# Kernel optimization log

Hardware: AMD Instinct MI355X
Metric: run time of the kernel (lower is better)

The kernel has to match this reference:

```python
import jax, jax.numpy as jnp
import numpy as np

B, N_TOKENS, E = 64, 512, 512   # batch, document tokens, embedding_dim
MAX_SEQ_LEN = 64                # decode steps


def setup_inputs() -> dict:
    key = jax.random.key(0)
    ks = jax.random.split(key, 11)
    s = 0.05
    return {
        "token_embeddings": jax.random.normal(ks[0], (B, N_TOKENS, 2 * E), jnp.float32),
        "encoded_document": jax.random.normal(ks[1], (B, 2 * E), jnp.float32),
        # LSTMCell params (hidden state is zero every step, so W_hh is dead; biases still add)
        "W_ih": jax.random.normal(ks[2], (4 * E, 2 * E), jnp.float32) * s,
        "b_ih": jax.random.normal(ks[3], (4 * E,), jnp.float32) * s,
        "b_hh": jax.random.normal(ks[4], (4 * E,), jnp.float32) * s,
        # decoder_weights: Linear(E, E)
        "Wd": jax.random.normal(ks[5], (E, E), jnp.float32) * s,
        "bd": jax.random.normal(ks[6], (E,), jnp.float32) * s,
        # encoder_weights: Linear(2E, E)
        "We": jax.random.normal(ks[7], (E, 2 * E), jnp.float32) * s,
        "be": jax.random.normal(ks[8], (E,), jnp.float32) * s,
        # reference: Linear(E, 1)
        "wr": jax.random.normal(ks[9], (1, E), jnp.float32) * s,
        "br": jax.random.normal(ks[10], (1,), jnp.float32) * s,
    }


def reference(token_embeddings, encoded_document, W_ih, b_ih, b_hh, Wd, bd, We, be, wr, br):
    b = token_embeddings.shape[0]
    batch_idx = jnp.arange(b)
    # encoder projection is loop-invariant: hoist it (same math as per-step recompute)
    enc = jnp.einsum('bnd,ed->bne', token_embeddings, We) + be  # [B, N, E]

    def lstm_zero_state(x):
        # PyTorch LSTMCell with default (zero) h, c each call
        gates = x @ W_ih.T + b_ih + b_hh  # [B, 4E]
        i, f, g, o = jnp.split(gates, 4, axis=-1)
        c = jax.nn.sigmoid(i) * jnp.tanh(g)
        return jax.nn.sigmoid(o) * jnp.tanh(c)

    def step(dec_in, _):
        hx = lstm_zero_state(dec_in)              # [B, E]
        q = hx @ Wd.T + bd                        # [B, E]
        comp = jnp.tanh(q[:, None, :] + enc)      # [B, N, E]
        scores = jnp.einsum('bne,e->bn', comp, wr[0]) + br[0]  # [B, N]
        logp = jax.nn.log_softmax(scores, axis=1)
        idx = jnp.argmax(logp, axis=1)            # [B]
        nxt = token_embeddings[batch_idx, idx]    # [B, 2E]
        return nxt, (logp, idx)

    _, (probs, idxs) = jax.lax.scan(step, encoded_document, None, length=MAX_SEQ_LEN)
    overall_probabilities = jnp.transpose(probs, (1, 0, 2))  # [B, MAX_SEQ_LEN, N]
    peak_indices = idxs.T                                     # [B, MAX_SEQ_LEN]
    return overall_probabilities, peak_indices
```

## Files before the change

### kernel.cpp

```cpp
#include <hip/hip_runtime.h>


#define DEV __device__ __forceinline__

DEV float sigm(float x) { return __fdividef(1.0f, 1.0f + __expf(-x)); }
DEV float tanh_fast(float x) {
  float e = __expf(2.0f * x);
  return 1.0f - __fdividef(2.0f, e + 1.0f);
}

#define FMA4(acc, xv, wv)                                                      \
  acc = fmaf((xv).x, (wv).x, acc); acc = fmaf((xv).y, (wv).y, acc);            \
  acc = fmaf((xv).z, (wv).z, acc); acc = fmaf((xv).w, (wv).w, acc)

__global__ __launch_bounds__(256) void kenc(const float* __restrict__ A,
                                            const float* __restrict__ Bm,
                                            const float* __restrict__ bias,
                                            float* __restrict__ C) {
  __shared__ float a_s[16][132];
  __shared__ float b_s[16][132];
  const int t = threadIdx.x;
  const int row = t >> 1;
  const int kq = (t & 1) * 8;
  const float* Arow = A + (blockIdx.x * 128 + row) * 1024 + kq;
  const float* Brow = Bm + (blockIdx.y * 128 + row) * 1024 + kq;
  const int tx = t & 15, ty = t >> 4;
  float acc[8][8] = {};
  for (int k0 = 0; k0 < 1024; k0 += 16) {
    float4 av0 = *(const float4*)(Arow + k0);
    float4 av1 = *(const float4*)(Arow + k0 + 4);
    float4 bv0 = *(const float4*)(Brow + k0);
    float4 bv1 = *(const float4*)(Brow + k0 + 4);
    __syncthreads();
    a_s[kq+0][row]=av0.x; a_s[kq+1][row]=av0.y; a_s[kq+2][row]=av0.z; a_s[kq+3][row]=av0.w;
    a_s[kq+4][row]=av1.x; a_s[kq+5][row]=av1.y; a_s[kq+6][row]=av1.z; a_s[kq+7][row]=av1.w;
    b_s[kq+0][row]=bv0.x; b_s[kq+1][row]=bv0.y; b_s[kq+2][row]=bv0.z; b_s[kq+3][row]=bv0.w;
    b_s[kq+4][row]=bv1.x; b_s[kq+5][row]=bv1.y; b_s[kq+6][row]=bv1.z; b_s[kq+7][row]=bv1.w;
    __syncthreads();
    #pragma unroll
    for (int k = 0; k < 16; ++k) {
      float a[8], b[8];
      *(float4*)(a)   = *(const float4*)&a_s[k][ty*8];
      *(float4*)(a+4) = *(const float4*)&a_s[k][ty*8+4];
      *(float4*)(b)   = *(const float4*)&b_s[k][tx*8];
      *(float4*)(b+4) = *(const float4*)&b_s[k][tx*8+4];
      #pragma unroll
      for (int i = 0; i < 8; ++i)
        #pragma unroll
        for (int j = 0; j < 8; ++j)
          acc[i][j] = fmaf(a[i], b[j], acc[i][j]);
    }
  }
  const int mb = blockIdx.x * 128 + ty * 8;
  const int eb = blockIdx.y * 128 + tx * 8;
  float bv[8];
  #pragma unroll
  for (int j = 0; j < 8; ++j) bv[j] = bias[eb + j];
  #pragma unroll
  for (int i = 0; i < 8; ++i) {
    float* orow = C + (mb + i) * 512 + eb;
    float4 o0, o1;
    o0.x=acc[i][0]+bv[0]; o0.y=acc[i][1]+bv[1]; o0.z=acc[i][2]+bv[2]; o0.w=acc[i][3]+bv[3];
    o1.x=acc[i][4]+bv[4]; o1.y=acc[i][5]+bv[5]; o1.z=acc[i][6]+bv[6]; o1.w=acc[i][7]+bv[7];
    *(float4*)orow = o0; *(float4*)(orow + 4) = o1;
  }
}

__global__ __launch_bounds__(256) void kstep_hx(
    const float* __restrict__ TE, const float* __restrict__ encd,
    const float* __restrict__ W_ih, const float* __restrict__ b_ih,
    const float* __restrict__ b_hh, const float* __restrict__ scores,
    float* __restrict__ hx, float* __restrict__ out_logp,
    float* __restrict__ out_idx, int step) {
  __shared__ int   idx_s[64];
  __shared__ float mx_s[64];
  __shared__ float wsum_s[4];
  __shared__ float part_s[4][64][6];
  const int g = blockIdx.x;
  const int t = threadIdx.x;
  const int lane = t & 63;
  const int wu = __builtin_amdgcn_readfirstlane(t >> 6);

  if (step > 0) {
    const int row = t >> 2, qq = t & 3;
    const float* srow = scores + row * 512;
    float bv = -3.0e38f; int bi = 0;
    #pragma unroll 8
    for (int n = qq; n < 512; n += 4) {
      float s = srow[n];
      if (s > bv) { bv = s; bi = n; }
    }
    #pragma unroll
    for (int m = 1; m <= 2; m <<= 1) {
      float ov = __shfl_xor(bv, m);
      int   oi = __shfl_xor(bi, m);
      if (ov > bv || (ov == bv && oi < bi)) { bv = ov; bi = oi; }
    }
    if (qq == 0) { idx_s[row] = bi; mx_s[row] = bv; }
  }
  __syncthreads();

  if (step > 0 && g < 64) {
    const float* srow = scores + g * 512;
    const float mx = mx_s[g];
    float ssum = __expf(srow[t] - mx) + __expf(srow[t + 256] - mx);
    #pragma unroll
    for (int m = 1; m <= 32; m <<= 1) ssum += __shfl_xor(ssum, m);
    if (lane == 0) wsum_s[wu] = ssum;
  }
  __syncthreads();
  if (step > 0 && g < 64) {
    const float* srow = scores + g * 512;
    const float lse = mx_s[g] + __logf(wsum_s[0] + wsum_s[1] + wsum_s[2] + wsum_s[3]);
    float* orow = out_logp + (g * 64 + (step - 1)) * 512;
    orow[t]       = srow[t]       - lse;
    orow[t + 256] = srow[t + 256] - lse;
    if (t == 0) out_idx[g * 64 + (step - 1)] = (float)idx_s[g];
  }

  const int k0 = 2 * g, k1 = 2 * g + 1;
  const int dbase = wu * 256;
  const float* p0 = W_ih + (k0        ) * 1024 + dbase;
  const float* p1 = W_ih + (k1        ) * 1024 + dbase;
  const float* p2 = W_ih + (1024 + k0) * 1024 + dbase;
  const float* p3 = W_ih + (1024 + k1) * 1024 + dbase;
  const float* p4 = W_ih + (1536 + k0) * 1024 + dbase;
  const float* p5 = W_ih + (1536 + k1) * 1024 + dbase;
  const float* xr = (step == 0) ? (encd + lane * 1024 + dbase)
                                : (TE + (lane * 512 + idx_s[lane]) * 1024 + dbase);
  float a0=0, a1=0, a2=0, a3=0, a4=0, a5=0;
  #pragma unroll 4
  for (int d = 0; d < 256; d += 4) {
    float4 xv = *(const float4*)(xr + d);
    float4 v0 = *(const float4*)(p0 + d);
    float4 v1 = *(const float4*)(p1 + d);
    float4 v2 = *(const float4*)(p2 + d);
    float4 v3 = *(const float4*)(p3 + d);
    float4 v4 = *(const float4*)(p4 + d);
    float4 v5 = *(const float4*)(p5 + d);
    FMA4(a0, xv, v0); FMA4(a1, xv, v1); FMA4(a2, xv, v2);
    FMA4(a3, xv, v3); FMA4(a4, xv, v4); FMA4(a5, xv, v5);
  }
  part_s[wu][lane][0]=a0; part_s[wu][lane][1]=a1; part_s[wu][lane][2]=a2;
  part_s[wu][lane][3]=a3; part_s[wu][lane][4]=a4; part_s[wu][lane][5]=a5;
  __syncthreads();

  if (t < 64) {
    float s0=0, s1=0, s2=0, s3=0, s4=0, s5=0;
    #pragma unroll
    for (int u = 0; u < 4; ++u) {
      s0 += part_s[u][t][0]; s1 += part_s[u][t][1]; s2 += part_s[u][t][2];
      s3 += part_s[u][t][3]; s4 += part_s[u][t][4]; s5 += part_s[u][t][5];
    }
    const float gi0 = s0 + b_ih[k0] + b_hh[k0];
    const float gi1 = s1 + b_ih[k1] + b_hh[k1];
    const float gg0 = s2 + b_ih[1024 + k0] + b_hh[1024 + k0];
    const float gg1 = s3 + b_ih[1024 + k1] + b_hh[1024 + k1];
    const float go0 = s4 + b_ih[1536 + k0] + b_hh[1536 + k0];
    const float go1 = s5 + b_ih[1536 + k1] + b_hh[1536 + k1];
    const float c0 = sigm(gi0) * tanh_fast(gg0);
    const float c1 = sigm(gi1) * tanh_fast(gg1);
    hx[t * 512 + k0] = sigm(go0) * tanh_fast(c0);
    hx[t * 512 + k1] = sigm(go1) * tanh_fast(c1);
  }
}

__global__ __launch_bounds__(256) void kq(const float* __restrict__ hx,
                                          const float* __restrict__ Wd,
                                          const float* __restrict__ bd,
                                          float* __restrict__ q) {
  __shared__ float part_s[4][64][4];
  const int g = blockIdx.x;
  const int t = threadIdx.x, lane = t & 63;
  const int wu = __builtin_amdgcn_readfirstlane(t >> 6);
  const int dbase = wu * 128;
  const int e0 = g * 4;
  const float* w0 = Wd + (e0 + 0) * 512 + dbase;
  const float* w1 = Wd + (e0 + 1) * 512 + dbase;
  const float* w2 = Wd + (e0 + 2) * 512 + dbase;
  const float* w3 = Wd + (e0 + 3) * 512 + dbase;
  const float* xr = hx + lane * 512 + dbase;
  float a0=0, a1=0, a2=0, a3=0;
  #pragma unroll 8
  for (int d = 0; d < 128; d += 4) {
    float4 xv = *(const float4*)(xr + d);
    float4 v0 = *(const float4*)(w0 + d);
    float4 v1 = *(const float4*)(w1 + d);
    float4 v2 = *(const float4*)(w2 + d);
    float4 v3 = *(const float4*)(w3 + d);
    FMA4(a0, xv, v0); FMA4(a1, xv, v1); FMA4(a2, xv, v2); FMA4(a3, xv, v3);
  }
  part_s[wu][lane][0]=a0; part_s[wu][lane][1]=a1;
  part_s[wu][lane][2]=a2; part_s[wu][lane][3]=a3;
  __syncthreads();
  if (t < 64) {
    float4 r;
    r.x = part_s[0][t][0]+part_s[1][t][0]+part_s[2][t][0]+part_s[3][t][0] + bd[e0+0];
    r.y = part_s[0][t][1]+part_s[1][t][1]+part_s[2][t][1]+part_s[3][t][1] + bd[e0+1];
    r.z = part_s[0][t][2]+part_s[1][t][2]+part_s[2][t][2]+part_s[3][t][2] + bd[e0+2];
    r.w = part_s[0][t][3]+part_s[1][t][3]+part_s[2][t][3]+part_s[3][t][3] + bd[e0+3];
    *(float4*)(q + t * 512 + e0) = r;
  }
}

__global__ __launch_bounds__(256) void kscore(const float* __restrict__ enc,
                                              const float* __restrict__ q,
                                              const float* __restrict__ wr,
                                              const float* __restrict__ br,
                                              float* __restrict__ scores) {
  const int bid = blockIdx.x;
  const int b = bid >> 3, c = bid & 7;
  const int t = threadIdx.x, lane = t & 63, w = t >> 6;
  const int le = lane & 15, nl = lane >> 4;
  float4 qv[8], wv[8];
  const float* qrow = q + b * 512 + le * 4;
  const float* wrp  = wr + le * 4;
  #pragma unroll
  for (int j = 0; j < 8; ++j) {
    qv[j] = *(const float4*)(qrow + 64 * j);
    wv[j] = *(const float4*)(wrp  + 64 * j);
  }
  const float brv = br[0];
  #pragma unroll
  for (int i = 0; i < 4; ++i) {
    const int n = c * 64 + w * 16 + i * 4 + nl;
    const float* erow = enc + (b * 512 + n) * 512 + le * 4;
    float acc = 0.0f;
    #pragma unroll
    for (int j = 0; j < 8; ++j) {
      float4 ev = *(const float4*)(erow + 64 * j);
      acc += wv[j].x * tanh_fast(qv[j].x + ev.x);
      acc += wv[j].y * tanh_fast(qv[j].y + ev.y);
      acc += wv[j].z * tanh_fast(qv[j].z + ev.z);
      acc += wv[j].w * tanh_fast(qv[j].w + ev.w);
    }
    acc += __shfl_xor(acc, 1);
    acc += __shfl_xor(acc, 2);
    acc += __shfl_xor(acc, 4);
    acc += __shfl_xor(acc, 8);
    if (le == 0) scores[b * 512 + n] = acc + brv;
  }
}

__global__ __launch_bounds__(256) void kfin(const float* __restrict__ scores,
                                            float* __restrict__ out_logp,
                                            float* __restrict__ out_idx) {
  __shared__ float mxw[4]; __shared__ int idw[4]; __shared__ float sw[4];
  const int b = blockIdx.x, t = threadIdx.x, lane = t & 63, w = t >> 6;
  const float* srow = scores + b * 512;
  const float s1 = srow[t], s2 = srow[t + 256];
  float bv; int bi;
  if (s1 >= s2) { bv = s1; bi = t; } else { bv = s2; bi = t + 256; }
  #pragma unroll
  for (int m = 1; m <= 32; m <<= 1) {
    float ov = __shfl_xor(bv, m);
    int   oi = __shfl_xor(bi, m);
    if (ov > bv || (ov == bv && oi < bi)) { bv = ov; bi = oi; }
  }
  if (lane == 0) { mxw[w] = bv; idw[w] = bi; }
  __syncthreads();
  float mx = mxw[0]; int mi = idw[0];
  #pragma unroll
  for (int u = 1; u < 4; ++u)
    if (mxw[u] > mx || (mxw[u] == mx && idw[u] < mi)) { mx = mxw[u]; mi = idw[u]; }
  float ssum = __expf(s1 - mx) + __expf(s2 - mx);
  #pragma unroll
  for (int m = 1; m <= 32; m <<= 1) ssum += __shfl_xor(ssum, m);
  if (lane == 0) sw[w] = ssum;
  __syncthreads();
  const float lse = mx + __logf(sw[0] + sw[1] + sw[2] + sw[3]);
  float* orow = out_logp + (b * 64 + 63) * 512;
  orow[t]       = s1 - lse;
  orow[t + 256] = s2 - lse;
  if (t == 0) out_idx[b * 64 + 63] = (float)mi;
}

extern "C" void kernel_launch(void* const* d_in, const int* in_sizes, int n_in,
                              void* d_out, int out_size, void* d_ws, size_t ws_size,
                              hipStream_t stream) {
  const float* TE   = (const float*)d_in[0];
  const float* encd = (const float*)d_in[1];
  const float* W_ih = (const float*)d_in[2];
  const float* b_ih = (const float*)d_in[3];
  const float* b_hh = (const float*)d_in[4];
  const float* Wd   = (const float*)d_in[5];
  const float* bd   = (const float*)d_in[6];
  const float* We   = (const float*)d_in[7];
  const float* be   = (const float*)d_in[8];
  const float* wr   = (const float*)d_in[9];
  const float* br   = (const float*)d_in[10];

  float* out     = (float*)d_out;
  float* out_idx = out + 64 * 64 * 512;

  float* enc    = (float*)d_ws;
  float* scores = enc + 16777216;
  float* hx     = scores + 32768;
  float* q      = hx + 32768;

  kenc<<<dim3(256, 4), 256, 0, stream>>>(TE, We, be, enc);
  for (int t = 0; t < 64; ++t) {
    kstep_hx<<<256, 256, 0, stream>>>(TE, encd, W_ih, b_ih, b_hh, scores, hx,
                                      out, out_idx, t);
    kq<<<128, 256, 0, stream>>>(hx, Wd, bd, q);
    kscore<<<512, 256, 0, stream>>>(enc, q, wr, br, scores);
  }
  kfin<<<64, 256, 0, stream>>>(scores, out, out_idx);
}
```

Measured before the change: 3.762 ms.

## Fuse argmax into score kernel via packed atomics, simplify tanh, resplit grids

The score kernel now computes each row's max and argmax by packing score and index into a 64-bit key and using shared-memory and global atomicMax. The step kernel then just reads that result instead of rescanning the whole score matrix in every block. The tanh-weighted sum is rewritten as sum(w) - 2*sum(w/(exp2(2x*log2e)+1)), which saves a subtract per element. The kq and kscore grids are doubled with half the work per block, and the kenc GEMM shared-memory read pattern is changed to strided 4-wide chunks to reduce bank conflicts. The changes to the argmax tie-break and to tanh rounding could slightly alter the chosen indices.

```diff
diff --git a/kernel.cpp b/kernel.cpp
--- a/kernel.cpp
+++ b/kernel.cpp
@@ -8,6 +8,18 @@
   float e = __expf(2.0f * x);
   return 1.0f - __fdividef(2.0f, e + 1.0f);
 }
+
+DEV unsigned long long pack_score(float s, int n) {
+  unsigned u = __float_as_uint(s);
+  unsigned key = (u & 0x80000000u) ? ~u : (u | 0x80000000u);
+  return ((unsigned long long)key << 32) | (unsigned)(511 - n);
+}
+DEV float unpack_score(unsigned long long p) {
+  unsigned key = (unsigned)(p >> 32);
+  unsigned u = (key & 0x80000000u) ? (key & 0x7fffffffu) : ~key;
+  return __uint_as_float(u);
+}
+DEV int unpack_idx(unsigned long long p) { return 511 - (int)(p & 0xffffu); }
 
 #define FMA4(acc, xv, wv)                                                      \
   acc = fmaf((xv).x, (wv).x, acc); acc = fmaf((xv).y, (wv).y, acc);            \
@@ -40,10 +52,10 @@
     #pragma unroll
     for (int k = 0; k < 16; ++k) {
       float a[8], b[8];
-      *(float4*)(a)   = *(const float4*)&a_s[k][ty*8];
-      *(float4*)(a+4) = *(const float4*)&a_s[k][ty*8+4];
-      *(float4*)(b)   = *(const float4*)&b_s[k][tx*8];
-      *(float4*)(b+4) = *(const float4*)&b_s[k][tx*8+4];
+      *(float4*)(a)   = *(const float4*)&a_s[k][ty*4];
+      *(float4*)(a+4) = *(const float4*)&a_s[k][64 + ty*4];
+      *(float4*)(b)   = *(const float4*)&b_s[k][tx*4];
+      *(float4*)(b+4) = *(const float4*)&b_s[k][64 + tx*4];
       #pragma unroll
       for (int i = 0; i < 8; ++i)
         #pragma unroll
@@ -51,25 +63,28 @@
           acc[i][j] = fmaf(a[i], b[j], acc[i][j]);
     }
   }
-  const int mb = blockIdx.x * 128 + ty * 8;
-  const int eb = blockIdx.y * 128 + tx * 8;
-  float bv[8];
-  #pragma unroll
-  for (int j = 0; j < 8; ++j) bv[j] = bias[eb + j];
+  const int mb = blockIdx.x * 128;
+  const int eb = blockIdx.y * 128;
+  float4 bv0 = *(const float4*)&bias[eb + tx*4];
+  float4 bv1 = *(const float4*)&bias[eb + 64 + tx*4];
   #pragma unroll
   for (int i = 0; i < 8; ++i) {
-    float* orow = C + (mb + i) * 512 + eb;
+    const int r = mb + ((i < 4) ? (ty*4 + i) : (64 + ty*4 + (i - 4)));
+    float* orow = C + r * 512 + eb;
     float4 o0, o1;
-    o0.x=acc[i][0]+bv[0]; o0.y=acc[i][1]+bv[1]; o0.z=acc[i][2]+bv[2]; o0.w=acc[i][3]+bv[3];
-    o1.x=acc[i][4]+bv[4]; o1.y=acc[i][5]+bv[5]; o1.z=acc[i][6]+bv[6]; o1.w=acc[i][7]+bv[7];
-    *(float4*)orow = o0; *(float4*)(orow + 4) = o1;
-  }
-}
-
-__global__ __launch_bounds__(256) void kstep_hx(
+    o0.x=acc[i][0]+bv0.x; o0.y=acc[i][1]+bv0.y; o0.z=acc[i][2]+bv0.z; o0.w=acc[i][3]+bv0.w;
+    o1.x=acc[i][4]+bv1.x; o1.y=acc[i][5]+bv1.y; o1.z=acc[i][6]+bv1.z; o1.w=acc[i][7]+bv1.w;
+    *(float4*)(orow + tx*4) = o0;
+    *(float4*)(orow + 64 + tx*4) = o1;
+  }
+}
+
+__global__ __launch_bounds__(256) void kstep(
     const float* __restrict__ TE, const float* __restrict__ encd,
     const float* __restrict__ W_ih, const float* __restrict__ b_ih,
     const float* __restrict__ b_hh, const float* __restrict__ scores,
+    const unsigned long long* __restrict__ mprev,
+    unsigned long long* __restrict__ mcur,
     float* __restrict__ hx, float* __restrict__ out_logp,
     float* __restrict__ out_idx, int step) {
   __shared__ int   idx_s[64];
@@ -81,22 +96,12 @@
   const int lane = t & 63;
   const int wu = __builtin_amdgcn_readfirstlane(t >> 6);
 
-  if (step > 0) {
-    const int row = t >> 2, qq = t & 3;
-    const float* srow = scores + row * 512;
-    float bv = -3.0e38f; int bi = 0;
-    #pragma unroll 8
-    for (int n = qq; n < 512; n += 4) {
-      float s = srow[n];
-      if (s > bv) { bv = s; bi = n; }
-    }
-    #pragma unroll
-    for (int m = 1; m <= 2; m <<= 1) {
-      float ov = __shfl_xor(bv, m);
-      int   oi = __shfl_xor(bi, m);
-      if (ov > bv || (ov == bv && oi < bi)) { bv = ov; bi = oi; }
-    }
-    if (qq == 0) { idx_s[row] = bi; mx_s[row] = bv; }
+  if (g == 0 && t < 64) mcur[t] = 0ULL;
+
+  if (step > 0 && t < 64) {
+    unsigned long long p = mprev[t];
+    idx_s[t] = unpack_idx(p);
+    mx_s[t]  = unpack_score(p);
   }
   __syncthreads();
 
@@ -169,37 +174,30 @@
                                           const float* __restrict__ Wd,
                                           const float* __restrict__ bd,
                                           float* __restrict__ q) {
-  __shared__ float part_s[4][64][4];
+  __shared__ float part_s[4][64][2];
   const int g = blockIdx.x;
   const int t = threadIdx.x, lane = t & 63;
   const int wu = __builtin_amdgcn_readfirstlane(t >> 6);
   const int dbase = wu * 128;
-  const int e0 = g * 4;
+  const int e0 = g * 2;
   const float* w0 = Wd + (e0 + 0) * 512 + dbase;
   const float* w1 = Wd + (e0 + 1) * 512 + dbase;
-  const float* w2 = Wd + (e0 + 2) * 512 + dbase;
-  const float* w3 = Wd + (e0 + 3) * 512 + dbase;
   const float* xr = hx + lane * 512 + dbase;
-  float a0=0, a1=0, a2=0, a3=0;
+  float a0=0, a1=0;
   #pragma unroll 8
   for (int d = 0; d < 128; d += 4) {
     float4 xv = *(const float4*)(xr + d);
     float4 v0 = *(const float4*)(w0 + d);
     float4 v1 = *(const float4*)(w1 + d);
-    float4 v2 = *(const float4*)(w2 + d);
-    float4 v3 = *(const float4*)(w3 + d);
-    FMA4(a0, xv, v0); FMA4(a1, xv, v1); FMA4(a2, xv, v2); FMA4(a3, xv, v3);
+    FMA4(a0, xv, v0); FMA4(a1, xv, v1);
   }
   part_s[wu][lane][0]=a0; part_s[wu][lane][1]=a1;
-  part_s[wu][lane][2]=a2; part_s[wu][lane][3]=a3;
   __syncthreads();
   if (t < 64) {
-    float4 r;
+    float2 r;
     r.x = part_s[0][t][0]+part_s[1][t][0]+part_s[2][t][0]+part_s[3][t][0] + bd[e0+0];
     r.y = part_s[0][t][1]+part_s[1][t][1]+part_s[2][t][1]+part_s[3][t][1] + bd[e0+1];
-    r.z = part_s[0][t][2]+part_s[1][t][2]+part_s[2][t][2]+part_s[3][t][2] + bd[e0+2];
-    r.w = part_s[0][t][3]+part_s[1][t][3]+part_s[2][t][3]+part_s[3][t][3] + bd[e0+3];
-    *(float4*)(q + t * 512 + e0) = r;
+    *(float2*)(q + t * 512 + e0) = r;
   }
 }
 
@@ -207,62 +205,65 @@
                                               const float* __restrict__ q,
                                               const float* __restrict__ wr,
                                               const float* __restrict__ br,
-                                              float* __restrict__ scores) {
+                                              float* __restrict__ scores,
+                                              unsigned long long* __restrict__ mtop) {
+  __shared__ unsigned long long lmax;
   const int bid = blockIdx.x;
-  const int b = bid >> 3, c = bid & 7;
-  const int t = threadIdx.x, lane = t & 63, w = t >> 6;
+  const int b = bid >> 4, c = bid & 15;
+  const int t = threadIdx.x, lane = t & 63, wu = t >> 6;
   const int le = lane & 15, nl = lane >> 4;
-  float4 qv[8], wv[8];
+  if (t == 0) lmax = 0ULL;
+  const float C2 = 2.8853900817779268f;
+  float4 wv[8], cq[8];
   const float* qrow = q + b * 512 + le * 4;
   const float* wrp  = wr + le * 4;
+  float swv = 0.0f;
   #pragma unroll
   for (int j = 0; j < 8; ++j) {
-    qv[j] = *(const float4*)(qrow + 64 * j);
-    wv[j] = *(const float4*)(wrp  + 64 * j);
-  }
+    wv[j] = *(const float4*)(wrp + 64 * j);
+    swv += wv[j].x + wv[j].y + wv[j].z + wv[j].w;
+    float4 qv = *(const float4*)(qrow + 64 * j);
+    cq[j].x = C2*qv.x; cq[j].y = C2*qv.y; cq[j].z = C2*qv.z; cq[j].w = C2*qv.w;
+  }
+  swv += __shfl_xor(swv, 1); swv += __shfl_xor(swv, 2);
+  swv += __shfl_xor(swv, 4); swv += __shfl_xor(swv, 8);
   const float brv = br[0];
+  __syncthreads();
   #pragma unroll
-  for (int i = 0; i < 4; ++i) {
-    const int n = c * 64 + w * 16 + i * 4 + nl;
+  for (int i = 0; i < 2; ++i) {
+    const int n = c * 32 + wu * 8 + i * 4 + nl;
     const float* erow = enc + (b * 512 + n) * 512 + le * 4;
     float acc = 0.0f;
     #pragma unroll
     for (int j = 0; j < 8; ++j) {
       float4 ev = *(const float4*)(erow + 64 * j);
-      acc += wv[j].x * tanh_fast(qv[j].x + ev.x);
-      acc += wv[j].y * tanh_fast(qv[j].y + ev.y);
-      acc += wv[j].z * tanh_fast(qv[j].z + ev.z);
-      acc += wv[j].w * tanh_fast(qv[j].w + ev.w);
+      acc = fmaf(wv[j].x, __fdividef(1.0f, __builtin_exp2f(fmaf(C2, ev.x, cq[j].x)) + 1.0f), acc);
+      acc = fmaf(wv[j].y, __fdividef(1.0f, __builtin_exp2f(fmaf(C2, ev.y, cq[j].y)) + 1.0f), acc);
+      acc = fmaf(wv[j].z, __fdividef(1.0f, __builtin_exp2f(fmaf(C2, ev.z, cq[j].z)) + 1.0f), acc);
+      acc = fmaf(wv[j].w, __fdividef(1.0f, __builtin_exp2f(fmaf(C2, ev.w, cq[j].w)) + 1.0f), acc);
     }
-    acc += __shfl_xor(acc, 1);
-    acc += __shfl_xor(acc, 2);
-    acc += __shfl_xor(acc, 4);
-    acc += __shfl_xor(acc, 8);
-    if (le == 0) scores[b * 512 + n] = acc + brv;
-  }
+    acc += __shfl_xor(acc, 1); acc += __shfl_xor(acc, 2);
+    acc += __shfl_xor(acc, 4); acc += __shfl_xor(acc, 8);
+    if (le == 0) {
+      const float sc = swv - 2.0f * acc + brv;
+      scores[b * 512 + n] = sc;
+      atomicMax(&lmax, pack_score(sc, n));
+    }
+  }
+  __syncthreads();
+  if (t == 0) atomicMax(&mtop[b], lmax);
 }
 
 __global__ __launch_bounds__(256) void kfin(const float* __restrict__ scores,
+                                            const unsigned long long* __restrict__ mtop,
                                             float* __restrict__ out_logp,
                                             float* __restrict__ out_idx) {
-  __shared__ float mxw[4]; __shared__ int idw[4]; __shared__ float sw[4];
+  __shared__ float sw[4];
   const int b = blockIdx.x, t = threadIdx.x, lane = t & 63, w = t >> 6;
   const float* srow = scores + b * 512;
   const float s1 = srow[t], s2 = srow[t + 256];
-  float bv; int bi;
-  if (s1 >= s2) { bv = s1; bi = t; } else { bv = s2; bi = t + 256; }
-  #pragma unroll
-  for (int m = 1; m <= 32; m <<= 1) {
-    float ov = __shfl_xor(bv, m);
-    int   oi = __shfl_xor(bi, m);
-    if (ov > bv || (ov == bv && oi < bi)) { bv = ov; bi = oi; }
-  }
-  if (lane == 0) { mxw[w] = bv; idw[w] = bi; }
-  __syncthreads();
-  float mx = mxw[0]; int mi = idw[0];
-  #pragma unroll
-  for (int u = 1; u < 4; ++u)
-    if (mxw[u] > mx || (mxw[u] == mx && idw[u] < mi)) { mx = mxw[u]; mi = idw[u]; }
+  const unsigned long long p = mtop[b];
+  const float mx = unpack_score(p);
   float ssum = __expf(s1 - mx) + __expf(s2 - mx);
   #pragma unroll
   for (int m = 1; m <= 32; m <<= 1) ssum += __shfl_xor(ssum, m);
@@ -272,7 +273,7 @@
   float* orow = out_logp + (b * 64 + 63) * 512;
   orow[t]       = s1 - lse;
   orow[t + 256] = s2 - lse;
-  if (t == 0) out_idx[b * 64 + 63] = (float)mi;
+  if (t == 0) out_idx[b * 64 + 63] = (float)unpack_idx(p);
 }
 
 extern "C" void kernel_launch(void* const* d_in, const int* in_sizes, int n_in,
@@ -297,13 +298,17 @@
   float* scores = enc + 16777216;
   float* hx     = scores + 32768;
   float* q      = hx + 32768;
+  unsigned long long* mbuf0 = (unsigned long long*)(q + 32768);
+  unsigned long long* mbuf1 = mbuf0 + 64;
 
   kenc<<<dim3(256, 4), 256, 0, stream>>>(TE, We, be, enc);
   for (int t = 0; t < 64; ++t) {
-    kstep_hx<<<256, 256, 0, stream>>>(TE, encd, W_ih, b_ih, b_hh, scores, hx,
-                                      out, out_idx, t);
-    kq<<<128, 256, 0, stream>>>(hx, Wd, bd, q);
-    kscore<<<512, 256, 0, stream>>>(enc, q, wr, br, scores);
-  }
-  kfin<<<64, 256, 0, stream>>>(scores, out, out_idx);
-}
+    unsigned long long* mprev = (t & 1) ? mbuf0 : mbuf1;
+    unsigned long long* mcur  = (t & 1) ? mbuf1 : mbuf0;
+    kstep<<<256, 256, 0, stream>>>(TE, encd, W_ih, b_ih, b_hh, scores, mprev,
+                                   mcur, hx, out, out_idx, t);
+    kq<<<256, 256, 0, stream>>>(hx, Wd, bd, q);
+    kscore<<<1024, 256, 0, stream>>>(enc, q, wr, br, scores, mcur);
+  }
+  kfin<<<64, 256, 0, stream>>>(scores, mbuf1, out, out_idx);
+}
```

Result: faster. 3.111 ms (-17.3%).
